# Kernel optimization log

Hardware: AMD Instinct MI355X
Metric: run time of the kernel (lower is better)

Reference implementation:

```python
import jax, jax.numpy as jnp
import numpy as np

D_MODEL = 1024
NUM_HEADS = 16
HEAD_DIM = D_MODEL // NUM_HEADS
CHUNK = 2048
BATCH = 1
SEQ = 8192  # 4 chunks of 2048


def setup_inputs() -> dict:
    key = jax.random.key(0)
    ks = jax.random.split(key, 5)
    hidden_states = jax.random.normal(ks[0], (BATCH, SEQ, D_MODEL), dtype=jnp.float32)
    scale = 0.02
    Wq = jax.random.normal(ks[1], (D_MODEL, D_MODEL), dtype=jnp.float32) * scale
    Wk = jax.random.normal(ks[2], (D_MODEL, D_MODEL), dtype=jnp.float32) * scale
    Wv = jax.random.normal(ks[3], (D_MODEL, D_MODEL), dtype=jnp.float32) * scale
    Wo = jax.random.normal(ks[4], (D_MODEL, D_MODEL), dtype=jnp.float32) * scale
    return {"hidden_states": hidden_states, "Wq": Wq, "Wk": Wk, "Wv": Wv, "Wo": Wo}


def reference(hidden_states, Wq, Wk, Wv, Wo):
    # nn.Linear(bias=False): y = x @ W.T, with W stored as [out, in]
    B, S, D = hidden_states.shape
    H, hd, C = NUM_HEADS, HEAD_DIM, CHUNK
    Nc = S // C  # seq divisible by chunk_size for full chunks

    def split_heads(x):
        # [B,S,D] -> [B,H,Nc,C,hd]
        return x.reshape(B, S, H, hd).transpose(0, 2, 1, 3).reshape(B, H, Nc, C, hd)

    q = split_heads(hidden_states @ Wq.T)
    k = split_heads(hidden_states @ Wk.T)
    v = split_heads(hidden_states @ Wv.T)

    # ring_size == 1 (single device): attention is chunk-local, causal within each chunk
    scores = jnp.einsum('bhnqd,bhnkd->bhnqk', q, k) / np.sqrt(hd).astype(jnp.float32)
    causal = jnp.tril(jnp.ones((C, C), dtype=bool))
    scores = jnp.where(causal, scores, -jnp.inf)
    attn = jax.nn.softmax(scores, axis=-1)
    out = jnp.einsum('bhnqk,bhnkd->bhnqd', attn, v)

    # [B,H,Nc,C,hd] -> [B,S,D]
    out = out.reshape(B, H, S, hd).transpose(0, 2, 1, 3).reshape(B, S, D)
    return out @ Wo.T
```

## Files before the change

kernel.cpp:

```cpp
#include <hip/hip_runtime.h>
#include <stdint.h>

#define D_MODEL 1024
#define NHEADS 16
#define HDIM 64
#define CHUNK 2048
#define SEQ 8192
#define NCHUNK 4

typedef __attribute__((ext_vector_type(8))) short bf16x8;
typedef __attribute__((ext_vector_type(4))) float f32x4;

static __device__ __forceinline__ short f2bf(float f) {
    unsigned int u = __builtin_bit_cast(unsigned int, f);
    u = (u + 0x7FFFu + ((u >> 16) & 1u)) >> 16;
    return (short)u;
}

static __device__ __forceinline__ unsigned int pkbf(float a, float b) {
    unsigned int ua = __builtin_bit_cast(unsigned int, a) + 0x8000u;
    unsigned int ub = __builtin_bit_cast(unsigned int, b) + 0x8000u;
    return (ua >> 16) | (ub & 0xFFFF0000u);
}

static __device__ __forceinline__ void gl_lds16(const void* g, void* l) {
    __builtin_amdgcn_global_load_lds((__attribute__((address_space(1))) void*)g,
                                     (__attribute__((address_space(3))) void*)l,
                                     16, 0, 0);
}

__global__ void cvt_f32_bf16(const float* __restrict__ in, short* __restrict__ out, int n) {
    int i = (blockIdx.x * 256 + threadIdx.x) * 4;
    if (i >= n) return;
    float4 v = *(const float4*)(in + i);
    short4 o;
    o.x = f2bf(v.x); o.y = f2bf(v.y); o.z = f2bf(v.z); o.w = f2bf(v.w);
    *(short4*)(out + i) = o;
}

__global__ void cvt_w4(const float* __restrict__ Wq, const float* __restrict__ Wk,
                       const float* __restrict__ Wv, const float* __restrict__ Wo,
                       short* __restrict__ Wqkv, short* __restrict__ Wob) {
    const int nW = D_MODEL * D_MODEL;
    int b = blockIdx.x;
    int which = b >> 10;
    const float* src = (which == 0) ? Wq : (which == 1) ? Wk : (which == 2) ? Wv : Wo;
    short* dst = (which < 3) ? (Wqkv + which * nW) : Wob;
    int i = ((b & 1023) * 256 + threadIdx.x) * 4;
    float4 v = *(const float4*)(src + i);
    short4 o;
    o.x = f2bf(v.x); o.y = f2bf(v.y); o.z = f2bf(v.z); o.w = f2bf(v.w);
    *(short4*)(dst + i) = o;
}


#define GEMM_STAGE(ABUF, BBUF, K0)                                            \
    {                                                                         \
        _Pragma("unroll")                                                     \
        for (int j = 0; j < 4; ++j) {                                         \
            gl_lds16(A + (size_t)(rowBase + srow[j]) * K + (K0) + skc[j],     \
                     &ABUF[(j * 256 + tid) * 8]);                             \
            gl_lds16(B + (size_t)(colBase + srow[j]) * K + (K0) + skc[j],     \
                     &BBUF[(j * 256 + tid) * 8]);                             \
        }                                                                     \
    }

#define GEMM_COMPUTE(ABUF, BBUF)                                              \
    {                                                                         \
        _Pragma("unroll")                                                     \
        for (int hf = 0; hf < 2; ++hf) {                                      \
            bf16x8 af[4], bfr[4];                                             \
            _Pragma("unroll")                                                 \
            for (int mi = 0; mi < 4; ++mi) {                                  \
                int row = wr * 64 + mi * 16 + cl;                             \
                af[mi] = *(const bf16x8*)&ABUF[row * 64 + (((hf * 4 + quad) ^ (row & 7)) * 8)]; \
            }                                                                 \
            _Pragma("unroll")                                                 \
            for (int ni = 0; ni < 4; ++ni) {                                  \
                int row = wc * 64 + ni * 16 + cl;                             \
                bfr[ni] = *(const bf16x8*)&BBUF[row * 64 + (((hf * 4 + quad) ^ (row & 7)) * 8)]; \
            }                                                                 \
            _Pragma("unroll")                                                 \
            for (int mi = 0; mi < 4; ++mi)                                    \
                _Pragma("unroll")                                             \
                for (int ni = 0; ni < 4; ++ni)                                \
                    acc[mi][ni] = __builtin_amdgcn_mfma_f32_16x16x32_bf16(af[mi], bfr[ni], acc[mi][ni], 0, 0, 0); \
        }                                                                     \
    }

#define GEMM_PRE()                                                            \
    const int tid  = threadIdx.x;                                             \
    const int lane = tid & 63;                                                \
    const int w    = tid >> 6;                                                \
    const int wr   = w >> 1, wc = w & 1;                                      \
    const int rowBase = blockIdx.y * 128;                                     \
    const int colBase = blockIdx.x * 128;                                     \
    const int quad = lane >> 4;                                               \
    const int cl   = lane & 15;                                               \
    f32x4 acc[4][4];                                                          \
    _Pragma("unroll")                                                         \
    for (int i = 0; i < 4; ++i)                                               \
        _Pragma("unroll")                                                     \
        for (int j = 0; j < 4; ++j)                                           \
            acc[i][j] = (f32x4){0.f, 0.f, 0.f, 0.f};                          \
    int srow[4], skc[4];                                                      \
    _Pragma("unroll")                                                         \
    for (int j = 0; j < 4; ++j) {                                             \
        int s = j * 256 + tid;                                                \
        srow[j] = s >> 3;                                                     \
        skc[j]  = ((s & 7) ^ (srow[j] & 7)) * 8;                              \
    }                                                                         \
    GEMM_STAGE(Asa, Bsa, 0);                                                  \
    for (int k0 = 0; k0 < K; k0 += 128) {                                     \
        __syncthreads();                                                      \
        if (k0 + 64 < K) GEMM_STAGE(Asb, Bsb, k0 + 64);                       \
        GEMM_COMPUTE(Asa, Bsa);                                               \
        __syncthreads();                                                      \
        if (k0 + 128 < K) GEMM_STAGE(Asa, Bsa, k0 + 128);                     \
        GEMM_COMPUTE(Asb, Bsb);                                               \
    }

__global__ __launch_bounds__(256) void gemm_qkv(const short* __restrict__ A,
                                                const short* __restrict__ B,
                                                short* __restrict__ QK,
                                                short* __restrict__ VT) {
    __shared__ __align__(16) short Asa[128 * 64];
    __shared__ __align__(16) short Asb[128 * 64];
    __shared__ __align__(16) short Bsa[128 * 64];
    __shared__ __align__(16) short Bsb[128 * 64];
    const int K = D_MODEL;
    GEMM_PRE();

    if (colBase < 2048) {
        #pragma unroll
        for (int mi = 0; mi < 4; ++mi)
            #pragma unroll
            for (int ni = 0; ni < 4; ++ni)
                #pragma unroll
                for (int r = 0; r < 4; ++r) {
                    int row = rowBase + wr * 64 + mi * 16 + quad * 4 + r;
                    int col = colBase + wc * 64 + ni * 16 + cl;
                    QK[(size_t)row * 2048 + col] = f2bf(acc[mi][ni][r]);
                }
    } else {
        #pragma unroll
        for (int mi = 0; mi < 4; ++mi) {
            int row0 = rowBase + wr * 64 + mi * 16 + quad * 4;
            int n = row0 >> 11, key = row0 & 2047;
            #pragma unroll
            for (int ni = 0; ni < 4; ++ni) {
                int c3 = colBase - 2048 + wc * 64 + ni * 16 + cl;
                int h = c3 >> 6, d = c3 & 63;
                short4 o;
                o.x = f2bf(acc[mi][ni][0]);
                o.y = f2bf(acc[mi][ni][1]);
                o.z = f2bf(acc[mi][ni][2]);
                o.w = f2bf(acc[mi][ni][3]);
                *(short4*)(VT + (size_t)((h * NCHUNK + n) * HDIM + d) * CHUNK + key) = o;
            }
        }
    }
}

__global__ __launch_bounds__(256) void gemm_out(const short* __restrict__ A,
                                                const short* __restrict__ B,
                                                float* __restrict__ Cout,
                                                int M, int N, int K) {
    __shared__ __align__(16) short Asa[128 * 64];
    __shared__ __align__(16) short Asb[128 * 64];
    __shared__ __align__(16) short Bsa[128 * 64];
    __shared__ __align__(16) short Bsb[128 * 64];
    GEMM_PRE();

    #pragma unroll
    for (int mi = 0; mi < 4; ++mi)
        #pragma unroll
        for (int ni = 0; ni < 4; ++ni)
            #pragma unroll
            for (int r = 0; r < 4; ++r) {
                int row = rowBase + wr * 64 + mi * 16 + quad * 4 + r;
                int col = colBase + wc * 64 + ni * 16 + cl;
                Cout[(size_t)row * N + col] = acc[mi][ni][r];
            }
}


#define ATTN_STAGE(BUF, T)                                                   \
    {                                                                        \
        const int kb2_ = (T) * 128;                                          \
        _Pragma("unroll")                                                    \
        for (int j = 0; j < 4; ++j) {                                        \
            int s = j * 256 + tid;                                           \
            int row = s >> 3;                                                \
            int c = (s & 7) ^ (row & 7);                                     \
            gl_lds16(Kg + (size_t)(kb2_ + row) * 2048 + c * 8, &BUF[s * 8]); \
        }                                                                    \
        _Pragma("unroll")                                                    \
        for (int j = 0; j < 4; ++j) {                                        \
            int s = j * 256 + tid;                                           \
            int d = s >> 4;                                                  \
            int c = (s & 15) ^ (d & 15);                                     \
            gl_lds16(VTg + (size_t)d * CHUNK + kb2_ + c * 8,                 \
                     &BUF[8192 + s * 8]);                                    \
        }                                                                    \
    }

#define ATTN_COMPUTE(BUF, T)                                                  \
    {                                                                         \
        const int kb_ = (T) * 128;                                            \
        const bool last_ = ((T) == qi);                                       \
        _Pragma("unroll")                                                     \
        for (int st = 0; st < 2; ++st) {                                      \
            const int sb = s0 + st * 16;                                      \
            const int qrow = sb + cl;                                         \
            f32x4 sa[8];                                                      \
            _Pragma("unroll")                                                 \
            for (int kt = 0; kt < 8; ++kt) {                                  \
                int key16 = kt * 16 + cl;                                     \
                bf16x8 k0 = *(const bf16x8*)(&BUF[(key16 * 8 + (quad ^ (cl & 7))) * 8]);       \
                bf16x8 k1 = *(const bf16x8*)(&BUF[(key16 * 8 + ((4 + quad) ^ (cl & 7))) * 8]); \
                sa[kt] = __builtin_amdgcn_mfma_f32_16x16x32_bf16(k0, qf[st][0],                \
                             (f32x4){0.f, 0.f, 0.f, 0.f}, 0, 0, 0);           \
                sa[kt] = __builtin_amdgcn_mfma_f32_16x16x32_bf16(k1, qf[st][1], sa[kt], 0, 0, 0); \
            }                                                                 \
            if (last_) {                                                      \
                _Pragma("unroll")                                             \
                for (int kt = 0; kt < 8; ++kt) {                              \
                    int kbase = kb_ + kt * 16 + quad * 4;                     \
                    _Pragma("unroll")                                         \
                    for (int r = 0; r < 4; ++r)                               \
                        if (kbase + r > qrow) sa[kt][r] = -3.0e38f;           \
                }                                                             \
            }                                                                 \
            float mx = fmaxf(fmaxf(sa[0][0], sa[0][1]), fmaxf(sa[0][2], sa[0][3])); \
            _Pragma("unroll")                                                 \
            for (int kt = 1; kt < 8; ++kt)                                    \
                mx = fmaxf(mx, fmaxf(fmaxf(sa[kt][0], sa[kt][1]),             \
                                     fmaxf(sa[kt][2], sa[kt][3])));           \
            mx = fmaxf(mx, __shfl_xor(mx, 16));                               \
            mx = fmaxf(mx, __shfl_xor(mx, 32));                               \
            float mnew = fmaxf(m2[st], mx);                                   \
            float alpha = __builtin_amdgcn_exp2f((m2[st] - mnew) * cs);       \
            float nm = mnew * cs;                                             \
            m2[st] = mnew;                                                    \
            l2[st] *= alpha;                                                  \
            _Pragma("unroll")                                                 \
            for (int dt = 0; dt < 4; ++dt)                                    \
                _Pragma("unroll")                                             \
                for (int r = 0; r < 4; ++r) o_acc[st][dt][r] *= alpha;        \
            _Pragma("unroll")                                                 \
            for (int kt = 0; kt < 8; ++kt)                                    \
                _Pragma("unroll")                                             \
                for (int r = 0; r < 4; ++r)                                   \
                    sa[kt][r] = __builtin_amdgcn_exp2f(__builtin_fmaf(sa[kt][r], cs, -nm)); \
            bf16x8 pfr[4];                                                    \
            _Pragma("unroll")                                                 \
            for (int g = 0; g < 4; ++g) {                                     \
                uint4 pk;                                                     \
                pk.x = pkbf(sa[2 * g][0], sa[2 * g][1]);                      \
                pk.y = pkbf(sa[2 * g][2], sa[2 * g][3]);                      \
                pk.z = pkbf(sa[2 * g + 1][0], sa[2 * g + 1][1]);              \
                pk.w = pkbf(sa[2 * g + 1][2], sa[2 * g + 1][3]);              \
                pfr[g] = __builtin_bit_cast(bf16x8, pk);                      \
            }                                                                 \
            f32x4 rs = (f32x4){0.f, 0.f, 0.f, 0.f};                           \
            _Pragma("unroll")                                                 \
            for (int g = 0; g < 4; ++g)                                       \
                rs = __builtin_amdgcn_mfma_f32_16x16x32_bf16(ones, pfr[g], rs, 0, 0, 0); \
            l2[st] += rs[0];                                                  \
            _Pragma("unroll")                                                 \
            for (int dt = 0; dt < 4; ++dt) {                                  \
                _Pragma("unroll")                                             \
                for (int g = 0; g < 4; ++g) {                                 \
                    int c0 = 4 * g + (quad >> 1);                             \
                    int base = (dt * 16 + cl) * 16;                           \
                    int q4 = (quad & 1) * 4;                                  \
                    short4 va = *(const short4*)(&BUF[8192 + (base + (c0 ^ cl)) * 8 + q4]);       \
                    short4 vb = *(const short4*)(&BUF[8192 + (base + ((c0 + 2) ^ cl)) * 8 + q4]); \
                    bf16x8 vf = {va.x, va.y, va.z, va.w, vb.x, vb.y, vb.z, vb.w};                 \
                    o_acc[st][dt] = __builtin_amdgcn_mfma_f32_16x16x32_bf16(vf, pfr[g], o_acc[st][dt], 0, 0, 0); \
                }                                                             \
            }                                                                 \
        }                                                                     \
    }

__global__ __launch_bounds__(256, 2) void attn_kernel(const short* __restrict__ QK,
                                                      const short* __restrict__ VT,
                                                      short* __restrict__ O) {
    __shared__ __align__(16) short KVa[16384];
    __shared__ __align__(16) short KVb[16384];
    const int tid  = threadIdx.x;
    const int lane = tid & 63;
    const int w    = tid >> 6;
    const int quad = lane >> 4;
    const int cl   = lane & 15;
    const int h = blockIdx.z;
    const int n = blockIdx.y;
    const int qa = (blockIdx.x + blockIdx.y + blockIdx.z) & 7;

    const short* Qg  = QK + (size_t)n * CHUNK * 2048 + h * HDIM;
    const short* Kg  = QK + (size_t)n * CHUNK * 2048 + 1024 + h * HDIM;
    const short* VTg = VT + (size_t)(h * NCHUNK + n) * HDIM * CHUNK;

    bf16x8 ones;
    #pragma unroll
    for (int i = 0; i < 8; ++i) ones[i] = (short)0x3F80;

    const float cs = 0.18033688011f;

    for (int ph = 0; ph < 2; ++ph) {
        const int qi = ph ? 15 - qa : qa;
        const int qb0 = qi * 128;
        const int s0  = qb0 + w * 32;

        bf16x8 qf[2][2];
        #pragma unroll
        for (int st = 0; st < 2; ++st)
            #pragma unroll
            for (int hf = 0; hf < 2; ++hf)
                qf[st][hf] = *(const bf16x8*)(Qg + (size_t)(s0 + st * 16 + cl) * 2048 + hf * 32 + quad * 8);

        float m2[2], l2[2];
        f32x4 o_acc[2][4];
        #pragma unroll
        for (int st = 0; st < 2; ++st) {
            m2[st] = -3.0e38f;
            l2[st] = 0.f;
            #pragma unroll
            for (int dt = 0; dt < 4; ++dt) o_acc[st][dt] = (f32x4){0.f, 0.f, 0.f, 0.f};
        }

        const int ntiles = qi + 1;

        if (ph) __syncthreads();
        ATTN_STAGE(KVa, 0);
        int t = 0;
        for (;;) {
            __syncthreads();
            if (t + 1 < ntiles) ATTN_STAGE(KVb, t + 1);
            ATTN_COMPUTE(KVa, t);
            if (++t >= ntiles) break;
            __syncthreads();
            if (t + 1 < ntiles) ATTN_STAGE(KVa, t + 1);
            ATTN_COMPUTE(KVb, t);
            if (++t >= ntiles) break;
        }

        #pragma unroll
        for (int st = 0; st < 2; ++st) {
            float linv = __builtin_amdgcn_rcpf(l2[st]);
            size_t rowoff = ((size_t)n * CHUNK + s0 + st * 16 + cl) * D_MODEL + h * HDIM;
            #pragma unroll
            for (int dt = 0; dt < 4; ++dt) {
                short4 o;
                o.x = f2bf(o_acc[st][dt][0] * linv);
                o.y = f2bf(o_acc[st][dt][1] * linv);
                o.z = f2bf(o_acc[st][dt][2] * linv);
                o.w = f2bf(o_acc[st][dt][3] * linv);
                *(short4*)(O + rowoff + dt * 16 + quad * 4) = o;
            }
        }
    }
}

extern "C" void kernel_launch(void* const* d_in, const int* in_sizes, int n_in,
                              void* d_out, int out_size, void* d_ws, size_t ws_size,
                              hipStream_t stream) {
    const float* hs = (const float*)d_in[0];
    const float* Wq = (const float*)d_in[1];
    const float* Wk = (const float*)d_in[2];
    const float* Wv = (const float*)d_in[3];
    const float* Wo = (const float*)d_in[4];
    float* out = (float*)d_out;

    char* ws = (char*)d_ws;
    const size_t MB = 1024 * 1024;
    short* Xbf  = (short*)(ws);
    short* QKb  = (short*)(ws + 16 * MB);
    short* VT   = (short*)(ws + 48 * MB);
    short* Abf  = (short*)(ws + 64 * MB);
    short* Wqkv = (short*)(ws + 80 * MB);
    short* Wob  = (short*)(ws + 86 * MB);

    const int nHS = SEQ * D_MODEL;
    cvt_f32_bf16<<<nHS / 1024, 256, 0, stream>>>(hs, Xbf, nHS);
    cvt_w4<<<4096, 256, 0, stream>>>(Wq, Wk, Wv, Wo, Wqkv, Wob);

    gemm_qkv<<<dim3(24, 64), 256, 0, stream>>>(Xbf, Wqkv, QKb, VT);

    attn_kernel<<<dim3(8, NCHUNK, NHEADS), 256, 0, stream>>>(QKb, VT, Abf);

    gemm_out<<<dim3(8, 64), 256, 0, stream>>>(Abf, Wob, out, SEQ, D_MODEL, D_MODEL);
}
```

Measured before the change: 250.4 us.

## Split attention into one block per query tile with single LDS buffer and setprio

Each attention block now handles a single query tile instead of a pair of tiles (512 to 1024 blocks). Tiles are ordered heavy-first/light-interleaved via a linear grid index. Double-buffered K/V LDS staging is replaced with one buffer and two barriers per tile, halving LDS so launch bounds can rise to 4 blocks per CU. Wave priority is raised around MFMA sections to favor matrix issue across co-resident waves. The trade is losing the load/compute overlap inside a block in exchange for more blocks overlapping each other.

```diff
diff --git a/kernel.cpp b/kernel.cpp
--- a/kernel.cpp
+++ b/kernel.cpp
@@ -214,6 +214,7 @@
             const int sb = s0 + st * 16;                                      \
             const int qrow = sb + cl;                                         \
             f32x4 sa[8];                                                      \
+            __builtin_amdgcn_s_setprio(1);                                    \
             _Pragma("unroll")                                                 \
             for (int kt = 0; kt < 8; ++kt) {                                  \
                 int key16 = kt * 16 + cl;                                     \
@@ -223,6 +224,7 @@
                              (f32x4){0.f, 0.f, 0.f, 0.f}, 0, 0, 0);           \
                 sa[kt] = __builtin_amdgcn_mfma_f32_16x16x32_bf16(k1, qf[st][1], sa[kt], 0, 0, 0); \
             }                                                                 \
+            __builtin_amdgcn_s_setprio(0);                                    \
             if (last_) {                                                      \
                 _Pragma("unroll")                                             \
                 for (int kt = 0; kt < 8; ++kt) {                              \
@@ -263,6 +265,7 @@
                 pk.w = pkbf(sa[2 * g + 1][2], sa[2 * g + 1][3]);              \
                 pfr[g] = __builtin_bit_cast(bf16x8, pk);                      \
             }                                                                 \
+            __builtin_amdgcn_s_setprio(1);                                    \
             f32x4 rs = (f32x4){0.f, 0.f, 0.f, 0.f};                           \
             _Pragma("unroll")                                                 \
             for (int g = 0; g < 4; ++g)                                       \
@@ -281,22 +284,28 @@
                     o_acc[st][dt] = __builtin_amdgcn_mfma_f32_16x16x32_bf16(vf, pfr[g], o_acc[st][dt], 0, 0, 0); \
                 }                                                             \
             }                                                                 \
+            __builtin_amdgcn_s_setprio(0);                                    \
         }                                                                     \
     }
 
-__global__ __launch_bounds__(256, 2) void attn_kernel(const short* __restrict__ QK,
+__global__ __launch_bounds__(256, 4) void attn_kernel(const short* __restrict__ QK,
                                                       const short* __restrict__ VT,
                                                       short* __restrict__ O) {
-    __shared__ __align__(16) short KVa[16384];
-    __shared__ __align__(16) short KVb[16384];
+    __shared__ __align__(16) short KV[16384];
     const int tid  = threadIdx.x;
     const int lane = tid & 63;
     const int w    = tid >> 6;
     const int quad = lane >> 4;
     const int cl   = lane & 15;
-    const int h = blockIdx.z;
-    const int n = blockIdx.y;
-    const int qa = (blockIdx.x + blockIdx.y + blockIdx.z) & 7;
+
+    const int jb = blockIdx.x;
+    const int c  = jb >> 8;
+    const int r  = jb & 255;
+    const int h  = r & 15;
+    const int nt = r >> 4;
+    const int n  = nt & 3;
+    const int t4 = nt >> 2;
+    const int qi = (c == 0) ? t4 : (c == 1) ? 15 - t4 : (c == 2) ? t4 + 4 : 11 - t4;
 
     const short* Qg  = QK + (size_t)n * CHUNK * 2048 + h * HDIM;
     const short* Kg  = QK + (size_t)n * CHUNK * 2048 + 1024 + h * HDIM;
@@ -308,57 +317,46 @@
 
     const float cs = 0.18033688011f;
 
-    for (int ph = 0; ph < 2; ++ph) {
-        const int qi = ph ? 15 - qa : qa;
-        const int qb0 = qi * 128;
-        const int s0  = qb0 + w * 32;
-
-        bf16x8 qf[2][2];
-        #pragma unroll
-        for (int st = 0; st < 2; ++st)
-            #pragma unroll
-            for (int hf = 0; hf < 2; ++hf)
-                qf[st][hf] = *(const bf16x8*)(Qg + (size_t)(s0 + st * 16 + cl) * 2048 + hf * 32 + quad * 8);
-
-        float m2[2], l2[2];
-        f32x4 o_acc[2][4];
-        #pragma unroll
-        for (int st = 0; st < 2; ++st) {
-            m2[st] = -3.0e38f;
-            l2[st] = 0.f;
-            #pragma unroll
-            for (int dt = 0; dt < 4; ++dt) o_acc[st][dt] = (f32x4){0.f, 0.f, 0.f, 0.f};
-        }
-
-        const int ntiles = qi + 1;
-
-        if (ph) __syncthreads();
-        ATTN_STAGE(KVa, 0);
-        int t = 0;
-        for (;;) {
-            __syncthreads();
-            if (t + 1 < ntiles) ATTN_STAGE(KVb, t + 1);
-            ATTN_COMPUTE(KVa, t);
-            if (++t >= ntiles) break;
-            __syncthreads();
-            if (t + 1 < ntiles) ATTN_STAGE(KVa, t + 1);
-            ATTN_COMPUTE(KVb, t);
-            if (++t >= ntiles) break;
-        }
-
-        #pragma unroll
-        for (int st = 0; st < 2; ++st) {
-            float linv = __builtin_amdgcn_rcpf(l2[st]);
-            size_t rowoff = ((size_t)n * CHUNK + s0 + st * 16 + cl) * D_MODEL + h * HDIM;
-            #pragma unroll
-            for (int dt = 0; dt < 4; ++dt) {
-                short4 o;
-                o.x = f2bf(o_acc[st][dt][0] * linv);
-                o.y = f2bf(o_acc[st][dt][1] * linv);
-                o.z = f2bf(o_acc[st][dt][2] * linv);
-                o.w = f2bf(o_acc[st][dt][3] * linv);
-                *(short4*)(O + rowoff + dt * 16 + quad * 4) = o;
-            }
+    const int qb0 = qi * 128;
+    const int s0  = qb0 + w * 32;
+
+    bf16x8 qf[2][2];
+    #pragma unroll
+    for (int st = 0; st < 2; ++st)
+        #pragma unroll
+        for (int hf = 0; hf < 2; ++hf)
+            qf[st][hf] = *(const bf16x8*)(Qg + (size_t)(s0 + st * 16 + cl) * 2048 + hf * 32 + quad * 8);
+
+    float m2[2], l2[2];
+    f32x4 o_acc[2][4];
+    #pragma unroll
+    for (int st = 0; st < 2; ++st) {
+        m2[st] = -3.0e38f;
+        l2[st] = 0.f;
+        #pragma unroll
+        for (int dt = 0; dt < 4; ++dt) o_acc[st][dt] = (f32x4){0.f, 0.f, 0.f, 0.f};
+    }
+
+    const int ntiles = qi + 1;
+    for (int t = 0; t < ntiles; ++t) {
+        __syncthreads();
+        ATTN_STAGE(KV, t);
+        __syncthreads();
+        ATTN_COMPUTE(KV, t);
+    }
+
+    #pragma unroll
+    for (int st = 0; st < 2; ++st) {
+        float linv = __builtin_amdgcn_rcpf(l2[st]);
+        size_t rowoff = ((size_t)n * CHUNK + s0 + st * 16 + cl) * D_MODEL + h * HDIM;
+        #pragma unroll
+        for (int dt = 0; dt < 4; ++dt) {
+            short4 o;
+            o.x = f2bf(o_acc[st][dt][0] * linv);
+            o.y = f2bf(o_acc[st][dt][1] * linv);
+            o.z = f2bf(o_acc[st][dt][2] * linv);
+            o.w = f2bf(o_acc[st][dt][3] * linv);
+            *(short4*)(O + rowoff + dt * 16 + quad * 4) = o;
         }
     }
 }
@@ -388,7 +386,7 @@
 
     gemm_qkv<<<dim3(24, 64), 256, 0, stream>>>(Xbf, Wqkv, QKb, VT);
 
-    attn_kernel<<<dim3(8, NCHUNK, NHEADS), 256, 0, stream>>>(QKb, VT, Abf);
+    attn_kernel<<<dim3(1024), 256, 0, stream>>>(QKb, VT, Abf);
 
     gemm_out<<<dim3(8, 64), 256, 0, stream>>>(Abf, Wob, out, SEQ, D_MODEL, D_MODEL);
 }
```

Result: slower. 538.8 us (+115.1%).
